# Kernel optimization log

Hardware: AMD Instinct MI355X
Metric: run time of the kernel (lower is better)

## Reference

```python
import jax, jax.numpy as jnp
import numpy as np

ITERS = 10  # resonator iterations (iterations=10 in init_kwargs)

def _bipolar(key, shape):
    return jnp.where(jax.random.normal(key, shape) >= 0, 1.0, -1.0).astype(jnp.float32)

def setup_inputs() -> dict:
    key = jax.random.key(0)
    k1, k2, k3 = jax.random.split(key, 3)
    b, f, v, d = 64, 4, 256, 16384
    input_ = _bipolar(k1, (b, d))
    init_estimates = _bipolar(k2, (b, f, d))
    codebooks = _bipolar(k3, (f, v, d))
    return {"input": input_, "init_estimates": init_estimates, "codebooks": codebooks}

def _sign(x):
    # multiset quantize: bipolar sign (ties -> +1), matching MAP-VSA quantization
    return jnp.where(x >= 0, 1.0, -1.0).astype(x.dtype)

def reference(input, init_estimates, codebooks):
    """CONCURRENT resonator, SOFTWARE mode, activation=NONE, stoch=NONE.
    input: (b, d) bipolar; init_estimates: (b, f, d); codebooks: (f, v, d).
    For bipolar vectors: bind = elementwise *, inverse = identity, so
    multibind of all-but-factor-j equals (product over all f) * estimate_j
    (since e*e = 1). This replaces the roll+stack+multibind with one fused pass.
    """
    def step(est, _):
        total = jnp.prod(est, axis=-2, keepdims=True)        # (b, 1, d)
        inv_others = total * est                             # (b, f, d) product of other factors
        new_est = input[:, None, :] * inv_others             # unbind: (b, f, d)
        sim = jnp.einsum('bfd,fvd->bfv', new_est, codebooks) # dot_similarity
        # multiset(codebook, similarity, quantize=True): sign of similarity-weighted sum
        est_new = _sign(jnp.einsum('bfv,fvd->bfd', sim, codebooks))
        return est_new, None
    est, _ = jax.lax.scan(step, init_estimates, None, length=ITERS)
    # cleanup: argmax of |similarity| per factor (argmax_abs=True)
    sim = jnp.einsum('bfd,fvd->bfv', est, codebooks)
    outcome = jnp.argmax(jnp.abs(sim), axis=-1)              # (b, f) codeword indices
    return est, outcome
```

## Files before the change

kernel.cpp:

```cpp
#include <hip/hip_runtime.h>
#include <stdint.h>

typedef unsigned long long ull;
typedef unsigned short ushort_t;
typedef __attribute__((ext_vector_type(8))) short bf16x8;
typedef __attribute__((ext_vector_type(4))) float f32x4;


__global__ __launch_bounds__(1024) void pack_mega(
        const float* __restrict__ in, const float* __restrict__ est_f,
        const float* __restrict__ cb,
        ull* __restrict__ in_bits, ull* __restrict__ est_bits, ull* __restrict__ cbw) {
    int gw   = (int)((blockIdx.x * 1024 + threadIdx.x) >> 6);
    int lane = threadIdx.x & 63;
    if (gw < 16384) {
        float x = in[(size_t)gw * 64 + lane];
        ull m = __ballot(x < 0.0f);
        if (lane == 0) in_bits[gw] = m;
    } else if (gw < 81920) {
        int g = gw - 16384;
        float x = est_f[(size_t)g * 64 + lane];
        ull m = __ballot(x < 0.0f);
        if (lane == 0) est_bits[g] = m;
    } else {
        int g = gw - 81920;
        int w = g & 255, fv = g >> 8;
        float x = cb[(size_t)fv * 16384 + (size_t)w * 64 + lane];
        ull m = __ballot(x < 0.0f);
        if (lane == 0) cbw[(size_t)((fv >> 8) * 256 + w) * 256 + (fv & 255)] = m;
    }
}

__global__ __launch_bounds__(1024) void pack_cbT(const ull* __restrict__ cbw, ull* __restrict__ cbT) {
    int gw   = (int)((blockIdx.x * 1024 + threadIdx.x) >> 6);
    int lane = threadIdx.x & 63;
    int f = gw >> 16, rem = gw & 65535, j = rem >> 14, d = rem & 16383;
    ull w = cbw[(size_t)(f * 256 + (d >> 6)) * 256 + j * 64 + lane];
    ull m = __ballot((w >> (d & 63)) & 1ull);
    if (lane == 0) cbT[(size_t)(f * 4 + j) * 16384 + d] = m;
}

__device__ __forceinline__ ushort_t f2bf(int x) {
    return (ushort_t)(__float_as_uint((float)x) >> 16);
}

__global__ __launch_bounds__(1024) void simA2_kernel(
        const ull* __restrict__ in_bits, const ull* __restrict__ est_in,
        const ull* __restrict__ cbw, ushort_t* __restrict__ outq, int mode) {
    int bid = blockIdx.x;
    int f    = (bid & 7) >> 1;
    int sub  = (bid & 1) * 32 + (bid >> 3);
    int vblk = sub & 3, bblk = sub >> 2;

    __shared__ ull s_cw[64][257];
    __shared__ ull s_ne[4][257];
    __shared__ short s_p[4][4][64];

    int t = threadIdx.x;

    {
        int bl = t >> 8, w = t & 255;
        int b = bblk * 4 + bl;
        ull e0 = est_in[(size_t)(b * 4 + 0) * 256 + w];
        ull e1 = est_in[(size_t)(b * 4 + 1) * 256 + w];
        ull e2 = est_in[(size_t)(b * 4 + 2) * 256 + w];
        ull e3 = est_in[(size_t)(b * 4 + 3) * 256 + w];
        ull ef = (f == 0) ? e0 : ((f == 1) ? e1 : ((f == 2) ? e2 : e3));
        ull val = mode ? ef
                       : (in_bits[(size_t)b * 256 + w] ^ e0 ^ e1 ^ e2 ^ e3 ^ ef);
        s_ne[bl][w] = val;
    }
    #pragma unroll 4
    for (int i = 0; i < 16; ++i) {
        int idx = i * 1024 + t;
        int v = idx & 63, w = idx >> 6;
        s_cw[v][w] = cbw[(size_t)(f * 256 + w) * 256 + vblk * 64 + v];
    }
    __syncthreads();

    {
        int lane = t & 63, wave = t >> 6;
        int bi = wave & 3, q = wave >> 2;
        int acc0 = 0, acc1 = 0;
        #pragma unroll 8
        for (int w = q * 64; w < q * 64 + 64; w += 2) {
            acc0 += __popcll(s_ne[bi][w]     ^ s_cw[lane][w]);
            acc1 += __popcll(s_ne[bi][w + 1] ^ s_cw[lane][w + 1]);
        }
        s_p[bi][q][lane] = (short)(acc0 + acc1);
    }
    __syncthreads();

    if (t < 256) {
        int bi = t >> 6, v2 = t & 63;
        int h = s_p[bi][0][v2] + s_p[bi][1][v2] + s_p[bi][2][v2] + s_p[bi][3][v2];
        int q16 = 16384 - h;
        int b = bblk * 4 + bi, v = vblk * 64 + v2;
        if (mode == 0) {
            size_t base = ((size_t)(f * 64 + b)) * 512 + v;
            outq[base]       = f2bf(q16 >> 8);
            outq[base + 256] = f2bf(q16 & 255);
        } else {
            outq[((size_t)(f * 64 + b)) * 256 + v] = (ushort_t)q16;
        }
    }
}

__global__ __launch_bounds__(512) void gemm_kernel(
        const ull* __restrict__ cbT, const ushort_t* __restrict__ simAB,
        ull* __restrict__ est_out) {
    int bid = blockIdx.x;
    int fB   = (bid & 7) >> 1;
    int dblk = (bid & 1) * 32 + (bid >> 3);
    __shared__ int4 sB[8192];
    __shared__ ull s_ball[8][8][4];
    __shared__ int s_off[256];
    int t = threadIdx.x, lane = t & 63, wave = t >> 6;

    if (t < 256) {
        int d = dblk * 256 + t;
        int npop = 0;
        #pragma unroll
        for (int j = 0; j < 4; ++j) npop += __popcll(cbT[((size_t)fB * 4 + j) * 16384 + d]);
        s_off[t] = 8192 * (256 - 2 * npop);
    }

    #pragma unroll 4
    for (int it = 0; it < 16; ++it) {
        int flat = it * 512 + t;
        int kc = flat >> 10, nt = (flat >> 6) & 15, l = flat & 63;
        int v0 = kc * 32 + ((l >> 4) << 3);
        int d  = dblk * 256 + nt * 16 + (l & 15);
        ull w = cbT[((size_t)fB * 4 + (v0 >> 6)) * 16384 + d];
        unsigned bits = (unsigned)(w >> (v0 & 63)) & 0xFFu;
        int4 val;
        val.x = 0x3F803F80 | ((bits & 1u) << 15)        | ((bits & 2u) << 30);
        val.y = 0x3F803F80 | (((bits >> 2) & 1u) << 15) | (((bits >> 2) & 2u) << 30);
        val.z = 0x3F803F80 | (((bits >> 4) & 1u) << 15) | (((bits >> 4) & 2u) << 30);
        val.w = 0x3F803F80 | (((bits >> 6) & 1u) << 15) | (((bits >> 6) & 2u) << 30);
        sB[flat] = val;
    }

    int mw = wave & 3, ntb = (wave >> 2) << 3;
    const ushort_t* abase = simAB
        + ((size_t)(fB * 64 + mw * 16 + (lane & 15))) * 512 + ((lane >> 4) << 3);
    bf16x8 Ahi[8], Alo[8];
    #pragma unroll
    for (int kc = 0; kc < 8; ++kc) {
        Ahi[kc] = *(const bf16x8*)(abase + kc * 32);
        Alo[kc] = *(const bf16x8*)(abase + 256 + kc * 32);
    }
    __syncthreads();

    #pragma unroll 2
    for (int ntl = 0; ntl < 8; ++ntl) {
        int nt = ntb + ntl;
        f32x4 acch = {0.f, 0.f, 0.f, 0.f}, accl = {0.f, 0.f, 0.f, 0.f};
        #pragma unroll
        for (int kc = 0; kc < 8; ++kc) {
            bf16x8 B = *(const bf16x8*)&sB[(kc * 16 + nt) * 64 + lane];
            acch = __builtin_amdgcn_mfma_f32_16x16x32_bf16(Ahi[kc], B, acch, 0, 0, 0);
            accl = __builtin_amdgcn_mfma_f32_16x16x32_bf16(Alo[kc], B, accl, 0, 0, 0);
        }
        float offf = (float)s_off[nt * 16 + (lane & 15)];
        #pragma unroll
        for (int r = 0; r < 4; ++r) {
            float S = 256.0f * acch[r] + accl[r];
            ull m = __ballot(S < offf);
            if (lane == 0) s_ball[wave][nt & 7][r] = m;
        }
    }
    __syncthreads();

    if (t < 256) {
        int b = t >> 2, w4 = t & 3;
        int wv = (b >> 4) + ((w4 >= 2) ? 4 : 0);
        ull word = 0;
        #pragma unroll
        for (int k = 0; k < 4; ++k) {
            int nt = w4 * 4 + k;
            ull m = s_ball[wv][nt & 7][b & 3];
            word |= ((m >> (((b >> 2) & 3) * 16)) & 0xFFFFull) << (k * 16);
        }
        est_out[((size_t)(b * 4 + fB)) * 256 + dblk * 4 + w4] = word;
    }
}

__global__ __launch_bounds__(256) void final2_kernel(
        const ull* __restrict__ est, const ushort_t* __restrict__ simF,
        float* __restrict__ out) {
    int t = threadIdx.x;
    if (blockIdx.x < 256 && t < 64) {
        int b = blockIdx.x >> 2, f = blockIdx.x & 3;
        const ushort_t* sf = simF + ((size_t)(f * 64 + b)) * 256 + t * 4;
        int best_a = -1, best_v = 0;
        #pragma unroll
        for (int k = 0; k < 4; ++k) {
            int sim = 2 * (int)sf[k] - 16384;
            int a = sim < 0 ? -sim : sim;
            if (a > best_a) { best_a = a; best_v = t * 4 + k; }
        }
        #pragma unroll
        for (int off = 1; off < 64; off <<= 1) {
            int oa = __shfl_xor(best_a, off);
            int ov = __shfl_xor(best_v, off);
            if (oa > best_a || (oa == best_a && ov < best_v)) { best_a = oa; best_v = ov; }
        }
        if (t == 0) out[4194304 + b * 4 + f] = (float)best_v;
    }
    int flat = blockIdx.x * 2048 + t * 8;
    ull w = est[flat >> 6];
    unsigned bits = (unsigned)(w >> (flat & 63)) & 0xFFu;
    float4 lo, hi;
    lo.x = (bits & 1u)   ? -1.0f : 1.0f;
    lo.y = (bits & 2u)   ? -1.0f : 1.0f;
    lo.z = (bits & 4u)   ? -1.0f : 1.0f;
    lo.w = (bits & 8u)   ? -1.0f : 1.0f;
    hi.x = (bits & 16u)  ? -1.0f : 1.0f;
    hi.y = (bits & 32u)  ? -1.0f : 1.0f;
    hi.z = (bits & 64u)  ? -1.0f : 1.0f;
    hi.w = (bits & 128u) ? -1.0f : 1.0f;
    *(float4*)(out + flat)     = lo;
    *(float4*)(out + flat + 4) = hi;
}

extern "C" void kernel_launch(void* const* d_in, const int* in_sizes, int n_in,
                              void* d_out, int out_size, void* d_ws, size_t ws_size,
                              hipStream_t stream) {
    const float* input    = (const float*)d_in[0];
    const float* init_est = (const float*)d_in[1];
    const float* cb       = (const float*)d_in[2];
    float* out = (float*)d_out;
    char* ws = (char*)d_ws;

    ull* in_bits    = (ull*)(ws + 0);
    ull* est0       = (ull*)(ws + 131072);
    ull* est1       = (ull*)(ws + 655360);
    ull* cbw        = (ull*)(ws + 1179648);
    ull* cbT        = (ull*)(ws + 3276800);
    ushort_t* simAB = (ushort_t*)(ws + 5373952);
    ushort_t* simF  = simAB;

    pack_mega<<<21504, 1024, 0, stream>>>(input, init_est, cb, in_bits, est0, cbw);
    pack_cbT<<<16384, 1024, 0, stream>>>(cbw, cbT);

    ull* bufs[2] = { est0, est1 };
    for (int i = 0; i < 10; ++i) {
        simA2_kernel<<<256, 1024, 0, stream>>>(in_bits, bufs[i & 1], cbw, simAB, 0);
        gemm_kernel<<<256, 512, 0, stream>>>(cbT, simAB, bufs[(i & 1) ^ 1]);
    }
    simA2_kernel<<<256, 1024, 0, stream>>>(in_bits, est0, cbw, simF, 1);
    final2_kernel<<<2048, 256, 0, stream>>>(est0, simF, out);
}
```

Measured before the change: 363.4 us.

## Batch bit-packing per wave, fold similarity offset, and retile codeword LDS layout

The pack kernels now have each wave produce 16 packed words instead of one, cutting the grid size and per-word launch and ballot overhead. In the similarity kernel the codeword tile is stored [w][v] with no padding, so lanes read consecutive 64-bit entries. The similarity is emitted directly as the signed value 16384-2h, split into high and low bf16 halves. This lets the GEMM compare against zero and drop its per-column popcount offset computation. The sign-convention change spans two kernels and must stay consistent to remain correct.

```diff
diff --git a/kernel.cpp b/kernel.cpp
--- a/kernel.cpp
+++ b/kernel.cpp
@@ -11,40 +11,55 @@
         const float* __restrict__ in, const float* __restrict__ est_f,
         const float* __restrict__ cb,
         ull* __restrict__ in_bits, ull* __restrict__ est_bits, ull* __restrict__ cbw) {
-    int gw   = (int)((blockIdx.x * 1024 + threadIdx.x) >> 6);
+    int wid  = (int)((blockIdx.x * 1024 + threadIdx.x) >> 6);
     int lane = threadIdx.x & 63;
-    if (gw < 16384) {
-        float x = in[(size_t)gw * 64 + lane];
-        ull m = __ballot(x < 0.0f);
-        if (lane == 0) in_bits[gw] = m;
-    } else if (gw < 81920) {
-        int g = gw - 16384;
-        float x = est_f[(size_t)g * 64 + lane];
-        ull m = __ballot(x < 0.0f);
-        if (lane == 0) est_bits[g] = m;
-    } else {
-        int g = gw - 81920;
-        int w = g & 255, fv = g >> 8;
-        float x = cb[(size_t)fv * 16384 + (size_t)w * 64 + lane];
-        ull m = __ballot(x < 0.0f);
-        if (lane == 0) cbw[(size_t)((fv >> 8) * 256 + w) * 256 + (fv & 255)] = m;
+    int w0 = wid * 16;
+    const float* s;
+    int wloc;
+    if (w0 < 16384)      { s = in;    wloc = w0; }
+    else if (w0 < 81920) { s = est_f; wloc = w0 - 16384; }
+    else                 { s = cb;    wloc = w0 - 81920; }
+    ull ball[16];
+    #pragma unroll
+    for (int k = 0; k < 16; ++k) {
+        float x = s[(size_t)(wloc + k) * 64 + lane];
+        ball[k] = __ballot(x < 0.0f);
+    }
+    if (lane == 0) {
+        if (w0 < 16384) {
+            #pragma unroll
+            for (int k = 0; k < 16; ++k) in_bits[wloc + k] = ball[k];
+        } else if (w0 < 81920) {
+            #pragma unroll
+            for (int k = 0; k < 16; ++k) est_bits[wloc + k] = ball[k];
+        } else {
+            #pragma unroll
+            for (int k = 0; k < 16; ++k) {
+                int g = wloc + k;
+                int f = g >> 16, v = (g >> 8) & 255, w = g & 255;
+                cbw[(size_t)(f * 256 + w) * 256 + v] = ball[k];
+            }
+        }
     }
 }
 
 __global__ __launch_bounds__(1024) void pack_cbT(const ull* __restrict__ cbw, ull* __restrict__ cbT) {
-    int gw   = (int)((blockIdx.x * 1024 + threadIdx.x) >> 6);
+    int wid  = (int)((blockIdx.x * 1024 + threadIdx.x) >> 6);
     int lane = threadIdx.x & 63;
-    int f = gw >> 16, rem = gw & 65535, j = rem >> 14, d = rem & 16383;
-    ull w = cbw[(size_t)(f * 256 + (d >> 6)) * 256 + j * 64 + lane];
-    ull m = __ballot((w >> (d & 63)) & 1ull);
-    if (lane == 0) cbT[(size_t)(f * 4 + j) * 16384 + d] = m;
-}
-
-__device__ __forceinline__ ushort_t f2bf(int x) {
-    return (ushort_t)(__float_as_uint((float)x) >> 16);
-}
-
-__global__ __launch_bounds__(1024) void simA2_kernel(
+    int f = wid >> 12, j = (wid >> 10) & 3, w = (wid >> 2) & 255, s2 = wid & 3;
+    ull cw = cbw[(size_t)(f * 256 + w) * 256 + j * 64 + lane];
+    ull ball[16];
+    #pragma unroll
+    for (int k = 0; k < 16; ++k)
+        ball[k] = __ballot((cw >> (s2 * 16 + k)) & 1ull);
+    if (lane == 0) {
+        #pragma unroll
+        for (int k = 0; k < 16; ++k)
+            cbT[(size_t)(f * 4 + j) * 16384 + w * 64 + s2 * 16 + k] = ball[k];
+    }
+}
+
+__global__ __launch_bounds__(1024) void simA3_kernel(
         const ull* __restrict__ in_bits, const ull* __restrict__ est_in,
         const ull* __restrict__ cbw, ushort_t* __restrict__ outq, int mode) {
     int bid = blockIdx.x;
@@ -52,8 +67,8 @@
     int sub  = (bid & 1) * 32 + (bid >> 3);
     int vblk = sub & 3, bblk = sub >> 2;
 
-    __shared__ ull s_cw[64][257];
-    __shared__ ull s_ne[4][257];
+    __shared__ ull s_cw[256][64];
+    __shared__ ull s_ne[4][256];
     __shared__ short s_p[4][4][64];
 
     int t = threadIdx.x;
@@ -66,42 +81,40 @@
         ull e2 = est_in[(size_t)(b * 4 + 2) * 256 + w];
         ull e3 = est_in[(size_t)(b * 4 + 3) * 256 + w];
         ull ef = (f == 0) ? e0 : ((f == 1) ? e1 : ((f == 2) ? e2 : e3));
-        ull val = mode ? ef
-                       : (in_bits[(size_t)b * 256 + w] ^ e0 ^ e1 ^ e2 ^ e3 ^ ef);
-        s_ne[bl][w] = val;
+        s_ne[bl][w] = mode ? ef
+                           : (in_bits[(size_t)b * 256 + w] ^ e0 ^ e1 ^ e2 ^ e3 ^ ef);
     }
     #pragma unroll 4
     for (int i = 0; i < 16; ++i) {
         int idx = i * 1024 + t;
-        int v = idx & 63, w = idx >> 6;
-        s_cw[v][w] = cbw[(size_t)(f * 256 + w) * 256 + vblk * 64 + v];
+        int w = idx >> 6, v = idx & 63;
+        s_cw[w][v] = cbw[(size_t)(f * 256 + w) * 256 + vblk * 64 + v];
     }
     __syncthreads();
 
     {
         int lane = t & 63, wave = t >> 6;
         int bi = wave & 3, q = wave >> 2;
-        int acc0 = 0, acc1 = 0;
+        int acc = 0;
         #pragma unroll 8
-        for (int w = q * 64; w < q * 64 + 64; w += 2) {
-            acc0 += __popcll(s_ne[bi][w]     ^ s_cw[lane][w]);
-            acc1 += __popcll(s_ne[bi][w + 1] ^ s_cw[lane][w + 1]);
-        }
-        s_p[bi][q][lane] = (short)(acc0 + acc1);
+        for (int w = q * 64; w < q * 64 + 64; ++w)
+            acc += __popcll(s_ne[bi][w] ^ s_cw[w][lane]);
+        s_p[bi][q][lane] = (short)acc;
     }
     __syncthreads();
 
     if (t < 256) {
         int bi = t >> 6, v2 = t & 63;
         int h = s_p[bi][0][v2] + s_p[bi][1][v2] + s_p[bi][2][v2] + s_p[bi][3][v2];
-        int q16 = 16384 - h;
         int b = bblk * 4 + bi, v = vblk * 64 + v2;
         if (mode == 0) {
+            int sim = 16384 - 2 * h;
+            int sh = sim >> 8, sl = sim & 255;
             size_t base = ((size_t)(f * 64 + b)) * 512 + v;
-            outq[base]       = f2bf(q16 >> 8);
-            outq[base + 256] = f2bf(q16 & 255);
+            outq[base]       = (ushort_t)(__float_as_uint((float)sh) >> 16);
+            outq[base + 256] = (ushort_t)(__float_as_uint((float)sl) >> 16);
         } else {
-            outq[((size_t)(f * 64 + b)) * 256 + v] = (ushort_t)q16;
+            outq[((size_t)(f * 64 + b)) * 256 + v] = (ushort_t)(16384 - h);
         }
     }
 }
@@ -114,16 +127,7 @@
     int dblk = (bid & 1) * 32 + (bid >> 3);
     __shared__ int4 sB[8192];
     __shared__ ull s_ball[8][8][4];
-    __shared__ int s_off[256];
     int t = threadIdx.x, lane = t & 63, wave = t >> 6;
-
-    if (t < 256) {
-        int d = dblk * 256 + t;
-        int npop = 0;
-        #pragma unroll
-        for (int j = 0; j < 4; ++j) npop += __popcll(cbT[((size_t)fB * 4 + j) * 16384 + d]);
-        s_off[t] = 8192 * (256 - 2 * npop);
-    }
 
     #pragma unroll 4
     for (int it = 0; it < 16; ++it) {
@@ -162,11 +166,10 @@
             acch = __builtin_amdgcn_mfma_f32_16x16x32_bf16(Ahi[kc], B, acch, 0, 0, 0);
             accl = __builtin_amdgcn_mfma_f32_16x16x32_bf16(Alo[kc], B, accl, 0, 0, 0);
         }
-        float offf = (float)s_off[nt * 16 + (lane & 15)];
         #pragma unroll
         for (int r = 0; r < 4; ++r) {
             float S = 256.0f * acch[r] + accl[r];
-            ull m = __ballot(S < offf);
+            ull m = __ballot(S < 0.0f);
             if (lane == 0) s_ball[wave][nt & 7][r] = m;
         }
     }
@@ -241,14 +244,14 @@
     ushort_t* simAB = (ushort_t*)(ws + 5373952);
     ushort_t* simF  = simAB;
 
-    pack_mega<<<21504, 1024, 0, stream>>>(input, init_est, cb, in_bits, est0, cbw);
-    pack_cbT<<<16384, 1024, 0, stream>>>(cbw, cbT);
+    pack_mega<<<1344, 1024, 0, stream>>>(input, init_est, cb, in_bits, est0, cbw);
+    pack_cbT<<<1024, 1024, 0, stream>>>(cbw, cbT);
 
     ull* bufs[2] = { est0, est1 };
     for (int i = 0; i < 10; ++i) {
-        simA2_kernel<<<256, 1024, 0, stream>>>(in_bits, bufs[i & 1], cbw, simAB, 0);
+        simA3_kernel<<<256, 1024, 0, stream>>>(in_bits, bufs[i & 1], cbw, simAB, 0);
         gemm_kernel<<<256, 512, 0, stream>>>(cbT, simAB, bufs[(i & 1) ^ 1]);
     }
-    simA2_kernel<<<256, 1024, 0, stream>>>(in_bits, est0, cbw, simF, 1);
+    simA3_kernel<<<256, 1024, 0, stream>>>(in_bits, est0, cbw, simF, 1);
     final2_kernel<<<2048, 256, 0, stream>>>(est0, simF, out);
 }
```

Result: faster. 318.9 us (-12.2%).
